# Performance work log

Hardware: AMD Instinct MI355X
Metric: run time of the kernel (lower is better)

Reference implementation:

```python
import jax, jax.numpy as jnp
import numpy as np

B, N, D = 8192, 4, 2048
DFF = 4 * D
EPS = float(np.finfo(np.float32).eps)  # torch RMSNorm eps=None -> finfo eps
SK_ITERS = 20


def setup_inputs() -> dict:
    key = jax.random.key(0)
    ks = jax.random.split(key, 12)
    nd = N * D
    return {
        "x": jax.random.normal(ks[0], (B, N, D), jnp.float32),
        "rms_weight": jnp.ones((nd,), jnp.float32),
        "theta_pre": jax.random.normal(ks[1], (nd, N), jnp.float32) * 0.02,
        "theta_post": jax.random.normal(ks[2], (nd, N), jnp.float32) * 0.02,
        "theta_res": jax.random.normal(ks[3], (nd, N * N), jnp.float32) * 0.02,
        "alpha_pre": jnp.float32(0.01),
        "alpha_post": jnp.float32(0.01),
        "alpha_res": jnp.float32(0.01),
        "b_pre": jnp.ones((1, N), jnp.float32) / N,
        "b_post": jnp.ones((1, N), jnp.float32),
        "b_res": jnp.eye(N, dtype=jnp.float32),
        "W1": jax.random.normal(ks[4], (D, DFF), jnp.float32) * (1.0 / np.sqrt(D)),
        "b1": jnp.zeros((DFF,), jnp.float32),
        "W2": jax.random.normal(ks[5], (DFF, D), jnp.float32) * (1.0 / np.sqrt(DFF)),
        "b2": jnp.zeros((D,), jnp.float32),
    }


def _sinkhorn_knopp(m, t=SK_ITERS):
    m = jnp.exp(m)
    for _ in range(t):  # fixed small iteration count, unrolled under jit
        m = m / jnp.sum(m, axis=-1, keepdims=True)
        m = m / jnp.sum(m, axis=-2, keepdims=True)
    return m


def reference(x, rms_weight, theta_pre, theta_post, theta_res,
              alpha_pre, alpha_post, alpha_res, b_pre, b_post, b_res,
              W1, b1, W2, b2):
    b, n, d = x.shape
    xf = x.reshape(b, n * d)                                   # [b, n*d]
    # RMSNorm over the flattened n*d dim
    xn = xf * jax.lax.rsqrt(jnp.mean(xf * xf, axis=-1, keepdims=True) + EPS) * rms_weight
    H_pre = jax.nn.sigmoid(alpha_pre * (xn @ theta_pre) + b_pre)          # [b, n]
    H_post = 2.0 * jax.nn.sigmoid(alpha_post * (xn @ theta_post) + b_post)  # [b, n]
    H_res = alpha_res * (xn @ theta_res).reshape(b, n, n) + b_res          # [b, n, n]
    H_res = _sinkhorn_knopp(H_res)
    x_pre = jnp.einsum("bn,bnd->bd", H_pre, x)                 # (H_pre @ x).squeeze(1)
    # wrapped layer: MLP d -> 4d -> d with exact GELU
    H_bar = jax.nn.gelu(x_pre @ W1 + b1, approximate=False) @ W2 + b2      # [b, d]
    z_l = H_post[:, :, None] * H_bar[:, None, :]               # einsum bn,bd->bnd
    h_l = jnp.einsum("bnm,bmd->bnd", H_res, x)                 # H_res @ x
    return z_l + h_l
```

## Files before the change

### kernel.cpp

```cpp
#include <hip/hip_runtime.h>
#include <hip/hip_bf16.h>
#include <math.h>

typedef __attribute__((ext_vector_type(4))) float  float4v;
typedef __attribute__((ext_vector_type(8))) unsigned short ushort8v;
typedef __attribute__((ext_vector_type(4))) unsigned short ushort4v;
typedef __attribute__((ext_vector_type(8))) __bf16 bf16x8;

typedef __attribute__((address_space(3))) unsigned int       lds_u32;
typedef const __attribute__((address_space(1))) unsigned int glb_u32;

#define BB   8192
#define NN   4
#define DD   2048
#define ND   8192
#define DFF  8192
#define EPSF 1.1920928955078125e-07f
#define RPB  4

__device__ __forceinline__ unsigned short f2bf(float f) {
  union { float f; unsigned int u; } v; v.f = f;
  unsigned int u = v.u;
  u += 0x7FFFu + ((u >> 16) & 1u);
  return (unsigned short)(u >> 16);
}

__global__ __launch_bounds__(256) void row_stats_kernel(
    const float* __restrict__ x, const float* __restrict__ w,
    const float* __restrict__ th_pre, const float* __restrict__ th_post,
    const float* __restrict__ th_res,
    const float* __restrict__ a_pre, const float* __restrict__ a_post,
    const float* __restrict__ a_res,
    const float* __restrict__ b_pre, const float* __restrict__ b_post,
    const float* __restrict__ b_res,
    float* __restrict__ Hpre, float* __restrict__ Hpost, float* __restrict__ Hres)
{
  const int b0 = blockIdx.x * RPB;
  const int t = threadIdx.x;
  const float* xr = x + (size_t)b0 * ND;

  float acc[RPB][25];
#pragma unroll
  for (int r = 0; r < RPB; ++r)
#pragma unroll
    for (int c = 0; c < 25; ++c) acc[r][c] = 0.0f;

  const float4v* tp = (const float4v*)th_pre;
  const float4v* tq = (const float4v*)th_post;
  const float4v* tr = (const float4v*)th_res;

  for (int j = 0; j < ND / 256; ++j) {
    int i = j * 256 + t;
    float wv = w[i];
    float4v p  = tp[i];
    float4v q  = tq[i];
    float4v r0 = tr[i*4+0], r1 = tr[i*4+1], r2 = tr[i*4+2], r3 = tr[i*4+3];
#pragma unroll
    for (int r = 0; r < RPB; ++r) {
      float xv = xr[(size_t)r * ND + i];
      float xw = xv * wv;
      acc[r][0] += xv * xv;
      acc[r][1] += xw * p.x;  acc[r][2] += xw * p.y;
      acc[r][3] += xw * p.z;  acc[r][4] += xw * p.w;
      acc[r][5] += xw * q.x;  acc[r][6] += xw * q.y;
      acc[r][7] += xw * q.z;  acc[r][8] += xw * q.w;
      acc[r][9]  += xw * r0.x; acc[r][10] += xw * r0.y;
      acc[r][11] += xw * r0.z; acc[r][12] += xw * r0.w;
      acc[r][13] += xw * r1.x; acc[r][14] += xw * r1.y;
      acc[r][15] += xw * r1.z; acc[r][16] += xw * r1.w;
      acc[r][17] += xw * r2.x; acc[r][18] += xw * r2.y;
      acc[r][19] += xw * r2.z; acc[r][20] += xw * r2.w;
      acc[r][21] += xw * r3.x; acc[r][22] += xw * r3.y;
      acc[r][23] += xw * r3.z; acc[r][24] += xw * r3.w;
    }
  }

#pragma unroll
  for (int r = 0; r < RPB; ++r)
#pragma unroll
    for (int c = 0; c < 25; ++c) {
#pragma unroll
      for (int off = 32; off > 0; off >>= 1)
        acc[r][c] += __shfl_down(acc[r][c], off);
    }

  __shared__ float red[4][RPB * 25];
  __shared__ float s[RPB * 25];
  int lane = t & 63, wv4 = t >> 6;
  if (lane == 0) {
#pragma unroll
    for (int r = 0; r < RPB; ++r)
#pragma unroll
      for (int c = 0; c < 25; ++c) red[wv4][r * 25 + c] = acc[r][c];
  }
  __syncthreads();
  if (t < RPB * 25) s[t] = red[0][t] + red[1][t] + red[2][t] + red[3][t];
  __syncthreads();

  if (t < RPB) {
    const int b = b0 + t;
    const float* sv = &s[t * 25];
    float scale = rsqrtf(sv[0] / (float)ND + EPSF);
    float ap = a_pre[0], apo = a_post[0], ar = a_res[0];

#pragma unroll
    for (int n = 0; n < 4; ++n) {
      float vpre = ap * sv[1 + n] * scale + b_pre[n];
      Hpre[b * 4 + n] = 1.0f / (1.0f + expf(-vpre));
      float vpost = apo * sv[5 + n] * scale + b_post[n];
      Hpost[b * 4 + n] = 2.0f / (1.0f + expf(-vpost));
    }

    float m[16];
#pragma unroll
    for (int k = 0; k < 16; ++k)
      m[k] = expf(ar * sv[9 + k] * scale + b_res[k]);

    for (int it = 0; it < 20; ++it) {
#pragma unroll
      for (int n = 0; n < 4; ++n) {
        float rs = m[n*4] + m[n*4+1] + m[n*4+2] + m[n*4+3];
        float inv = 1.0f / rs;
        m[n*4] *= inv; m[n*4+1] *= inv; m[n*4+2] *= inv; m[n*4+3] *= inv;
      }
#pragma unroll
      for (int c = 0; c < 4; ++c) {
        float cs = m[c] + m[4+c] + m[8+c] + m[12+c];
        float inv = 1.0f / cs;
        m[c] *= inv; m[4+c] *= inv; m[8+c] *= inv; m[12+c] *= inv;
      }
    }
#pragma unroll
    for (int k = 0; k < 16; ++k) Hres[b * 16 + k] = m[k];
  }
}

__global__ __launch_bounds__(256) void xpre_kernel(
    const float* __restrict__ x, const float* __restrict__ Hpre,
    unsigned short* __restrict__ xpre)
{
  int b = blockIdx.x, t = threadIdx.x;
  float h0 = Hpre[b*4+0], h1 = Hpre[b*4+1], h2 = Hpre[b*4+2], h3 = Hpre[b*4+3];
  const float4v* xb = (const float4v*)(x + (size_t)b * ND);
  ushort4v* ob = (ushort4v*)(xpre + (size_t)b * DD);
#pragma unroll
  for (int g = 0; g < 2; ++g) {
    int i = g * 256 + t;
    float4v v = h0 * xb[i] + h1 * xb[512 + i] + h2 * xb[1024 + i] + h3 * xb[1536 + i];
    ushort4v o;
    o.x = f2bf(v.x); o.y = f2bf(v.y); o.z = f2bf(v.z); o.w = f2bf(v.w);
    ob[i] = o;
  }
}

__global__ __launch_bounds__(256) void transpose_bf16_kernel(
    const float* __restrict__ W, unsigned short* __restrict__ Wt, int K, int N)
{
  __shared__ float tile[64][65];
  int tx = threadIdx.x & 63, ty = threadIdx.x >> 6;
  int k0 = blockIdx.y * 64, n0 = blockIdx.x * 64;
#pragma unroll
  for (int r = 0; r < 16; ++r) {
    int kk = r * 4 + ty;
    tile[kk][tx] = W[(size_t)(k0 + kk) * N + n0 + tx];
  }
  __syncthreads();
#pragma unroll
  for (int r = 0; r < 16; ++r) {
    int nn = r * 4 + ty;
    Wt[(size_t)(n0 + nn) * K + k0 + tx] = f2bf(tile[tx][nn]);
  }
}

#define GBM 128
#define GBN 128
#define GBK 32

template<int EPI>
__global__ __launch_bounds__(256) void gemm_bf16(
    const unsigned short* __restrict__ A, const unsigned short* __restrict__ Bt,
    const float* __restrict__ bias, void* __restrict__ Cout,
    int M, int N, int K)
{
  __shared__ unsigned short As[GBM * GBK];
  __shared__ unsigned short Bs[GBN * GBK];

  const int t = threadIdx.x;
  const int lane = t & 63, wave = t >> 6;
  const int wm = wave >> 1, wn = wave & 1;
  const int m0 = blockIdx.y * GBM, n0 = blockIdx.x * GBN;

  float4v acc[4][4];
#pragma unroll
  for (int i = 0; i < 4; ++i)
#pragma unroll
    for (int j = 0; j < 4; ++j) acc[i][j] = (float4v)0.0f;

  const int srow = wave * 16 + (lane >> 2);
  const int skg  = (lane & 3) * 8;
  const unsigned short* Ag0 = A  + (size_t)(m0 + srow) * K + skg;
  const unsigned short* Ag1 = A  + (size_t)(m0 + srow + 64) * K + skg;
  const unsigned short* Bg0 = Bt + (size_t)(n0 + srow) * K + skg;
  const unsigned short* Bg1 = Bt + (size_t)(n0 + srow + 64) * K + skg;
  unsigned short* Al0 = &As[wave * 512];
  unsigned short* Al1 = &As[2048 + wave * 512];
  unsigned short* Bl0 = &Bs[wave * 512];
  unsigned short* Bl1 = &Bs[2048 + wave * 512];

  const int k0 = (lane >> 4) * 8;
  const int rr = lane & 15;

  for (int kt = 0; kt < K; kt += GBK) {
    __builtin_amdgcn_global_load_lds((glb_u32*)(Ag0 + kt), (lds_u32*)Al0, 16, 0, 0);
    __builtin_amdgcn_global_load_lds((glb_u32*)(Ag1 + kt), (lds_u32*)Al1, 16, 0, 0);
    __builtin_amdgcn_global_load_lds((glb_u32*)(Bg0 + kt), (lds_u32*)Bl0, 16, 0, 0);
    __builtin_amdgcn_global_load_lds((glb_u32*)(Bg1 + kt), (lds_u32*)Bl1, 16, 0, 0);
    __syncthreads();

    bf16x8 af[4], bfr[4];
#pragma unroll
    for (int i = 0; i < 4; ++i) {
      af[i]  = *reinterpret_cast<const bf16x8*>(&As[(wm * 64 + i * 16 + rr) * GBK + k0]);
      bfr[i] = *reinterpret_cast<const bf16x8*>(&Bs[(wn * 64 + i * 16 + rr) * GBK + k0]);
    }
#pragma unroll
    for (int mi = 0; mi < 4; ++mi)
#pragma unroll
      for (int ni = 0; ni < 4; ++ni)
        acc[mi][ni] = __builtin_amdgcn_mfma_f32_16x16x32_bf16(
            af[mi], bfr[ni], acc[mi][ni], 0, 0, 0);
    __syncthreads();
  }

  const int cl = lane & 15;
  const int rbase = (lane >> 4) * 4;
#pragma unroll
  for (int mi = 0; mi < 4; ++mi) {
#pragma unroll
    for (int ni = 0; ni < 4; ++ni) {
      int col = n0 + wn * 64 + ni * 16 + cl;
      float bv = bias[col];
#pragma unroll
      for (int r = 0; r < 4; ++r) {
        int row = m0 + wm * 64 + mi * 16 + rbase + r;
        float v = acc[mi][ni][r] + bv;
        if (EPI == 1) {
          v = 0.5f * v * (1.0f + erff(v * 0.70710678118654752f));
          ((unsigned short*)Cout)[(size_t)row * N + col] = f2bf(v);
        } else {
          ((float*)Cout)[(size_t)row * N + col] = v;
        }
      }
    }
  }
}

__global__ __launch_bounds__(256) void final_kernel(
    const float* __restrict__ x, const float* __restrict__ Hpost,
    const float* __restrict__ Hres, const float* __restrict__ Hbar,
    float* __restrict__ out)
{
  int b = blockIdx.x, t = threadIdx.x;
  float hp[4], hr[16];
#pragma unroll
  for (int n = 0; n < 4; ++n) hp[n] = Hpost[b * 4 + n];
#pragma unroll
  for (int k = 0; k < 16; ++k) hr[k] = Hres[b * 16 + k];

  const float4v* xb = (const float4v*)(x + (size_t)b * ND);
  const float4v* hb = (const float4v*)(Hbar + (size_t)b * DD);
  float4v* ob = (float4v*)(out + (size_t)b * ND);

#pragma unroll
  for (int g = 0; g < 2; ++g) {
    int i = g * 256 + t;
    float4v x0 = xb[i], x1 = xb[512 + i], x2 = xb[1024 + i], x3 = xb[1536 + i];
    float4v hv = hb[i];
#pragma unroll
    for (int n = 0; n < 4; ++n) {
      float4v o = hp[n] * hv
                + hr[n*4+0] * x0 + hr[n*4+1] * x1
                + hr[n*4+2] * x2 + hr[n*4+3] * x3;
      ob[n * 512 + i] = o;
    }
  }
}

extern "C" void kernel_launch(void* const* d_in, const int* in_sizes, int n_in,
                              void* d_out, int out_size, void* d_ws, size_t ws_size,
                              hipStream_t stream) {
  const float* x       = (const float*)d_in[0];
  const float* rms_w   = (const float*)d_in[1];
  const float* th_pre  = (const float*)d_in[2];
  const float* th_post = (const float*)d_in[3];
  const float* th_res  = (const float*)d_in[4];
  const float* a_pre   = (const float*)d_in[5];
  const float* a_post  = (const float*)d_in[6];
  const float* a_res   = (const float*)d_in[7];
  const float* b_pre   = (const float*)d_in[8];
  const float* b_post  = (const float*)d_in[9];
  const float* b_res   = (const float*)d_in[10];
  const float* W1      = (const float*)d_in[11];
  const float* b1      = (const float*)d_in[12];
  const float* W2      = (const float*)d_in[13];
  const float* b2      = (const float*)d_in[14];
  float* out = (float*)d_out;

  char* ws = (char*)d_ws;
  float* Hpre  = (float*)ws;                 ws += (size_t)BB * 4 * 4;
  float* Hpost = (float*)ws;                 ws += (size_t)BB * 4 * 4;
  float* Hres  = (float*)ws;                 ws += (size_t)BB * 16 * 4;
  unsigned short* xpre = (unsigned short*)ws; ws += (size_t)BB * DD * 2;
  unsigned short* W1t  = (unsigned short*)ws; ws += (size_t)DFF * DD * 2;
  unsigned short* W2t  = (unsigned short*)ws; ws += (size_t)DD * DFF * 2;
  unsigned short* G    = (unsigned short*)ws; ws += (size_t)BB * DFF * 2;
  float* Hbar = (float*)ws;                  ws += (size_t)BB * DD * 4;

  row_stats_kernel<<<dim3(BB / RPB), dim3(256), 0, stream>>>(
      x, rms_w, th_pre, th_post, th_res, a_pre, a_post, a_res,
      b_pre, b_post, b_res, Hpre, Hpost, Hres);

  xpre_kernel<<<dim3(BB), dim3(256), 0, stream>>>(x, Hpre, xpre);

  transpose_bf16_kernel<<<dim3(DFF / 64, DD / 64), dim3(256), 0, stream>>>(
      W1, W1t, DD, DFF);
  transpose_bf16_kernel<<<dim3(DD / 64, DFF / 64), dim3(256), 0, stream>>>(
      W2, W2t, DFF, DD);

  gemm_bf16<1><<<dim3(DFF / GBN, BB / GBM), dim3(256), 0, stream>>>(
      xpre, W1t, b1, (void*)G, BB, DFF, DD);

  gemm_bf16<0><<<dim3(DD / GBN, BB / GBM), dim3(256), 0, stream>>>(
      G, W2t, b2, (void*)Hbar, BB, DD, DFF);

  final_kernel<<<dim3(BB), dim3(256), 0, stream>>>(x, Hpost, Hres, Hbar, out);
}
```

Before: 1.613 ms.

## Replace 128x128 GEMM with pipelined 256x256 double-buffered swizzled MFMA kernel

Both MLP GEMMs move to a new kernel with 256x256 tiles, 512 threads and a 64-wide K step. It double-buffers LDS and loads straight from global into LDS, with XOR-swizzled layout to avoid bank conflicts. It also adds an interleaved load/MFMA schedule with explicit barriers, wait counts and setprio, plus a workgroup swizzle for L2 locality. The goal is more data reuse per tile and overlap of memory traffic with matrix-core work, at the cost of far more register and LDS use per block and a fragile hand-tuned schedule.

```diff
diff --git a/kernel.cpp b/kernel.cpp
--- a/kernel.cpp
+++ b/kernel.cpp
@@ -3,7 +3,6 @@
 #include <math.h>
 
 typedef __attribute__((ext_vector_type(4))) float  float4v;
-typedef __attribute__((ext_vector_type(8))) unsigned short ushort8v;
 typedef __attribute__((ext_vector_type(4))) unsigned short ushort4v;
 typedef __attribute__((ext_vector_type(8))) __bf16 bf16x8;
 
@@ -172,88 +171,187 @@
   }
 }
 
-#define GBM 128
-#define GBN 128
-#define GBK 32
-
-template<int EPI>
-__global__ __launch_bounds__(256) void gemm_bf16(
+
+#define STAGE_A(bb, h, kt) do { \
+    const unsigned short* _s = baseA + (size_t)((h) * 128) * KD + (size_t)(kt) * 64; \
+    __builtin_amdgcn_global_load_lds((glb_u32*)_s, \
+        (lds_u32*)(ldsA + ((bb) << 14) + ((h) << 13)), 16, 0, 0); \
+    __builtin_amdgcn_global_load_lds((glb_u32*)(_s + (size_t)64 * KD), \
+        (lds_u32*)(ldsA + ((bb) << 14) + ((h) << 13) + 4096), 16, 0, 0); \
+  } while (0)
+
+#define STAGE_B(bb, h, kt) do { \
+    const unsigned short* _s = baseB + (size_t)((h) * 128) * KD + (size_t)(kt) * 64; \
+    __builtin_amdgcn_global_load_lds((glb_u32*)_s, \
+        (lds_u32*)(ldsB + ((bb) << 14) + ((h) << 13)), 16, 0, 0); \
+    __builtin_amdgcn_global_load_lds((glb_u32*)(_s + (size_t)64 * KD), \
+        (lds_u32*)(ldsB + ((bb) << 14) + ((h) << 13) + 4096), 16, 0, 0); \
+  } while (0)
+
+#define LDSA(buf, mi, ks) (*reinterpret_cast<const bf16x8*>( \
+    AsB + ((buf) << 15) + aBase + ((mi) << 11) + (s0 ^ ((ks) << 6))))
+#define LDSB(buf, ni, ks) (*reinterpret_cast<const bf16x8*>( \
+    BsB + ((buf) << 15) + bBase + ((ni) << 11) + (s0 ^ ((ks) << 6))))
+
+#define RD_A0(buf) { _Pragma("unroll") for (int mi = 0; mi < 4; ++mi) { \
+    _Pragma("unroll") for (int ks = 0; ks < 2; ++ks) a0[mi][ks] = LDSA(buf, mi, ks); } }
+#define RD_A1(buf) { _Pragma("unroll") for (int mi = 0; mi < 4; ++mi) { \
+    _Pragma("unroll") for (int ks = 0; ks < 2; ++ks) a1[mi][ks] = LDSA(buf, 4 + mi, ks); } }
+#define RD_B0(buf) { _Pragma("unroll") for (int ni = 0; ni < 2; ++ni) { \
+    _Pragma("unroll") for (int ks = 0; ks < 2; ++ks) b0[ni][ks] = LDSB(buf, ni, ks); } }
+#define RD_B1(buf) { _Pragma("unroll") for (int ni = 0; ni < 2; ++ni) { \
+    _Pragma("unroll") for (int ks = 0; ks < 2; ++ks) b1[ni][ks] = LDSB(buf, 2 + ni, ks); } }
+
+#define QUAD(AF, BF, MB, NB) { \
+    __builtin_amdgcn_s_setprio(1); \
+    _Pragma("unroll") for (int m = 0; m < 4; ++m) { \
+      _Pragma("unroll") for (int n = 0; n < 2; ++n) { \
+        _Pragma("unroll") for (int ks = 0; ks < 2; ++ks) { \
+          acc[(MB) + m][(NB) + n] = __builtin_amdgcn_mfma_f32_16x16x32_bf16( \
+              AF[m][ks], BF[n][ks], acc[(MB) + m][(NB) + n], 0, 0, 0); } } } \
+    __builtin_amdgcn_s_setprio(0); }
+
+#define SBAR() do { __builtin_amdgcn_sched_barrier(0); \
+    __builtin_amdgcn_s_barrier(); __builtin_amdgcn_sched_barrier(0); } while (0)
+#define LGKM0() do { asm volatile("s_waitcnt lgkmcnt(0)" ::: "memory"); \
+    __builtin_amdgcn_sched_barrier(0); } while (0)
+#define VMC4() do { asm volatile("s_waitcnt vmcnt(4)" ::: "memory"); } while (0)
+
+template<int EPI, int KD, int NDim>
+__global__ __launch_bounds__(512, 2) void gemm256(
     const unsigned short* __restrict__ A, const unsigned short* __restrict__ Bt,
-    const float* __restrict__ bias, void* __restrict__ Cout,
-    int M, int N, int K)
+    const float* __restrict__ bias, void* __restrict__ Cout)
 {
-  __shared__ unsigned short As[GBM * GBK];
-  __shared__ unsigned short Bs[GBN * GBK];
+  __shared__ __align__(16) unsigned short As[2 * 16384];
+  __shared__ __align__(16) unsigned short Bs[2 * 16384];
 
   const int t = threadIdx.x;
   const int lane = t & 63, wave = t >> 6;
-  const int wm = wave >> 1, wn = wave & 1;
-  const int m0 = blockIdx.y * GBM, n0 = blockIdx.x * GBN;
-
-  float4v acc[4][4];
-#pragma unroll
-  for (int i = 0; i < 4; ++i)
+  const int wm = wave >> 2, wn = wave & 3;
+
+  constexpr int NBX = NDim / 256;
+  constexpr int NWG = NBX * (BB / 256);
+  constexpr int NT  = KD / 64;
+  constexpr int NIT = NT / 2;
+
+  const int lin = blockIdx.y * NBX + blockIdx.x;
+  const int swz = (lin & 7) * (NWG / 8) + (lin >> 3);
+  const int m0 = (swz / NBX) * 256;
+  const int n0 = (swz % NBX) * 256;
+
+  const int l8 = lane >> 3, l7 = lane & 7;
+  const unsigned short* baseA = A  + (size_t)(m0 + wave * 8 + l8) * KD + ((l7 ^ l8) << 3);
+  const unsigned short* baseB = Bt + (size_t)(n0 + wave * 8 + l8) * KD + ((l7 ^ l8) << 3);
+  unsigned short* ldsA = &As[wave * 512];
+  unsigned short* ldsB = &Bs[wave * 512];
+
+  const int rr = lane & 15, qq = lane >> 4;
+  const int s0 = (qq ^ (rr & 7)) << 4;
+  const char* AsB = (const char*)As;
+  const char* BsB = (const char*)Bs;
+  const int aBase = (wm << 14) + (rr << 7);
+  const int bBase = (wn << 13) + (rr << 7);
+
+  float4v acc[8][4];
+#pragma unroll
+  for (int i = 0; i < 8; ++i)
 #pragma unroll
     for (int j = 0; j < 4; ++j) acc[i][j] = (float4v)0.0f;
 
-  const int srow = wave * 16 + (lane >> 2);
-  const int skg  = (lane & 3) * 8;
-  const unsigned short* Ag0 = A  + (size_t)(m0 + srow) * K + skg;
-  const unsigned short* Ag1 = A  + (size_t)(m0 + srow + 64) * K + skg;
-  const unsigned short* Bg0 = Bt + (size_t)(n0 + srow) * K + skg;
-  const unsigned short* Bg1 = Bt + (size_t)(n0 + srow + 64) * K + skg;
-  unsigned short* Al0 = &As[wave * 512];
-  unsigned short* Al1 = &As[2048 + wave * 512];
-  unsigned short* Bl0 = &Bs[wave * 512];
-  unsigned short* Bl1 = &Bs[2048 + wave * 512];
-
-  const int k0 = (lane >> 4) * 8;
-  const int rr = lane & 15;
-
-  for (int kt = 0; kt < K; kt += GBK) {
-    __builtin_amdgcn_global_load_lds((glb_u32*)(Ag0 + kt), (lds_u32*)Al0, 16, 0, 0);
-    __builtin_amdgcn_global_load_lds((glb_u32*)(Ag1 + kt), (lds_u32*)Al1, 16, 0, 0);
-    __builtin_amdgcn_global_load_lds((glb_u32*)(Bg0 + kt), (lds_u32*)Bl0, 16, 0, 0);
-    __builtin_amdgcn_global_load_lds((glb_u32*)(Bg1 + kt), (lds_u32*)Bl1, 16, 0, 0);
-    __syncthreads();
-
-    bf16x8 af[4], bfr[4];
-#pragma unroll
-    for (int i = 0; i < 4; ++i) {
-      af[i]  = *reinterpret_cast<const bf16x8*>(&As[(wm * 64 + i * 16 + rr) * GBK + k0]);
-      bfr[i] = *reinterpret_cast<const bf16x8*>(&Bs[(wn * 64 + i * 16 + rr) * GBK + k0]);
-    }
-#pragma unroll
-    for (int mi = 0; mi < 4; ++mi)
-#pragma unroll
-      for (int ni = 0; ni < 4; ++ni)
-        acc[mi][ni] = __builtin_amdgcn_mfma_f32_16x16x32_bf16(
-            af[mi], bfr[ni], acc[mi][ni], 0, 0, 0);
-    __syncthreads();
+  bf16x8 a0[4][2], a1[4][2], b0[2][2], b1[2][2];
+
+  STAGE_B(0, 0, 0); STAGE_B(0, 1, 0);
+  STAGE_A(0, 0, 0); STAGE_A(0, 1, 0);
+  STAGE_B(1, 0, 1); STAGE_B(1, 1, 1);
+  VMC4();
+  SBAR();
+
+#pragma unroll 1
+  for (int i = 0; i < NIT; ++i) {
+    const int t1 = 2 * i + 1;
+    const int t2 = (2 * i + 2 < NT) ? 2 * i + 2 : NT - 1;
+    const int t3 = (2 * i + 3 < NT) ? 2 * i + 3 : NT - 1;
+
+    RD_A0(0); RD_B0(0);
+    STAGE_A(1, 0, t1);
+    SBAR(); LGKM0();
+    QUAD(a0, b0, 0, 0);
+    SBAR();
+    RD_B1(0);
+    STAGE_A(1, 1, t1);
+    SBAR(); LGKM0();
+    QUAD(a0, b1, 0, 2);
+    SBAR();
+    RD_A1(0);
+    STAGE_B(0, 0, t2);
+    SBAR(); LGKM0();
+    QUAD(a1, b0, 4, 0);
+    SBAR();
+    STAGE_B(0, 1, t2);
+    SBAR(); LGKM0();
+    QUAD(a1, b1, 4, 2);
+    VMC4();
+    SBAR();
+    RD_A0(1); RD_B0(1);
+    STAGE_A(0, 0, t2);
+    SBAR(); LGKM0();
+    QUAD(a0, b0, 0, 0);
+    SBAR();
+    RD_B1(1);
+    STAGE_A(0, 1, t2);
+    SBAR(); LGKM0();
+    QUAD(a0, b1, 0, 2);
+    SBAR();
+    RD_A1(1);
+    STAGE_B(1, 0, t3);
+    SBAR(); LGKM0();
+    QUAD(a1, b0, 4, 0);
+    SBAR();
+    STAGE_B(1, 1, t3);
+    SBAR(); LGKM0();
+    QUAD(a1, b1, 4, 2);
+    VMC4();
+    SBAR();
   }
 
   const int cl = lane & 15;
-  const int rbase = (lane >> 4) * 4;
-#pragma unroll
-  for (int mi = 0; mi < 4; ++mi) {
+  const int colB = n0 + wn * 64 + cl;
+  const int rowB = m0 + wm * 128 + (lane >> 4) * 4;
+  float bv[4];
+#pragma unroll
+  for (int ni = 0; ni < 4; ++ni) bv[ni] = bias[colB + ni * 16];
+#pragma unroll
+  for (int mi = 0; mi < 8; ++mi) {
 #pragma unroll
     for (int ni = 0; ni < 4; ++ni) {
-      int col = n0 + wn * 64 + ni * 16 + cl;
-      float bv = bias[col];
 #pragma unroll
       for (int r = 0; r < 4; ++r) {
-        int row = m0 + wm * 64 + mi * 16 + rbase + r;
-        float v = acc[mi][ni][r] + bv;
+        int row = rowB + mi * 16 + r;
+        int col = colB + ni * 16;
+        float v = acc[mi][ni][r] + bv[ni];
         if (EPI == 1) {
           v = 0.5f * v * (1.0f + erff(v * 0.70710678118654752f));
-          ((unsigned short*)Cout)[(size_t)row * N + col] = f2bf(v);
+          ((unsigned short*)Cout)[(size_t)row * NDim + col] = f2bf(v);
         } else {
-          ((float*)Cout)[(size_t)row * N + col] = v;
+          ((float*)Cout)[(size_t)row * NDim + col] = v;
         }
       }
     }
   }
 }
+
+#undef STAGE_A
+#undef STAGE_B
+#undef LDSA
+#undef LDSB
+#undef RD_A0
+#undef RD_A1
+#undef RD_B0
+#undef RD_B1
+#undef QUAD
+#undef SBAR
+#undef LGKM0
+#undef VMC4
 
 __global__ __launch_bounds__(256) void final_kernel(
     const float* __restrict__ x, const float* __restrict__ Hpost,
@@ -327,11 +425,11 @@
   transpose_bf16_kernel<<<dim3(DD / 64, DFF / 64), dim3(256), 0, stream>>>(
       W2, W2t, DFF, DD);
 
-  gemm_bf16<1><<<dim3(DFF / GBN, BB / GBM), dim3(256), 0, stream>>>(
-      xpre, W1t, b1, (void*)G, BB, DFF, DD);
-
-  gemm_bf16<0><<<dim3(DD / GBN, BB / GBM), dim3(256), 0, stream>>>(
-      G, W2t, b2, (void*)Hbar, BB, DD, DFF);
+  gemm256<1, DD, DFF><<<dim3(DFF / 256, BB / 256), dim3(512), 0, stream>>>(
+      xpre, W1t, b1, (void*)G);
+
+  gemm256<0, DFF, DD><<<dim3(DD / 256, BB / 256), dim3(512), 0, stream>>>(
+      G, W2t, b2, (void*)Hbar);
 
   final_kernel<<<dim3(BB), dim3(256), 0, stream>>>(x, Hpost, Hres, Hbar, out);
 }
```

After: 1.312 ms. 1.23x faster.
